# Performance work log

Measured on AMD Instinct MI355X. Metric: run time of the kernel, lower is better.

Reference implementation:

```python
import jax, jax.numpy as jnp
import numpy as np

B, T, D_IN, H, D_OUT = 256, 512, 64, 256, 8


def setup_inputs() -> dict:
    key = jax.random.key(0)
    ks = jax.random.split(key, 6)
    s_ih = 1.0 / np.sqrt(H)
    inputs = jax.random.normal(ks[0], (B, T, D_IN), dtype=jnp.float32)
    h0 = jnp.zeros((B, H), dtype=jnp.float32)
    c0 = jnp.zeros((B, H), dtype=jnp.float32)
    # LSTM cell params, PyTorch gate order (i, f, g, o)
    W_ih = jax.random.uniform(ks[1], (4 * H, D_IN), minval=-s_ih, maxval=s_ih, dtype=jnp.float32)
    W_hh = jax.random.uniform(ks[2], (4 * H, H), minval=-s_ih, maxval=s_ih, dtype=jnp.float32)
    b = jax.random.uniform(ks[3], (4 * H,), minval=-s_ih, maxval=s_ih, dtype=jnp.float32)
    # output projection (xavier_uniform weight, zero bias)
    lim = np.sqrt(6.0 / (H + D_OUT))
    W_out = jax.random.uniform(ks[4], (D_OUT, H), minval=-lim, maxval=lim, dtype=jnp.float32)
    b_out = jnp.zeros((D_OUT,), dtype=jnp.float32)
    return {"inputs": inputs, "h0": h0, "c0": c0, "W_ih": W_ih, "W_hh": W_hh,
            "b": b, "W_out": W_out, "b_out": b_out}


def _lstm_last(inputs, h0, c0, W_ih, W_hh, b):
    # inputs: [B, T, D_in] -> scan over time, keep only final hidden state
    xs = jnp.swapaxes(inputs, 0, 1)  # [T, B, D_in]

    def step(carry, x_t):
        h, c = carry
        gates = x_t @ W_ih.T + h @ W_hh.T + b  # [B, 4H]
        i, f, g, o = jnp.split(gates, 4, axis=-1)
        c_new = jax.nn.sigmoid(f) * c + jax.nn.sigmoid(i) * jnp.tanh(g)
        h_new = jax.nn.sigmoid(o) * jnp.tanh(c_new)
        return (h_new, c_new), None

    (h, c), _ = jax.lax.scan(step, (h0, c0), xs)
    return h, c


def reference(inputs, h0, c0, W_ih, W_hh, b, W_out, b_out):
    h, c = _lstm_last(inputs, h0, c0, W_ih, W_hh, b)
    rnn_outputs = h  # last-timestep output (dropout_prob=0 -> identity)
    logits = rnn_outputs @ W_out.T + b_out
    return (rnn_outputs, logits, h, c)
```

## Files before the change

### kernel.cpp

```cpp
#include <hip/hip_runtime.h>

#define T_ 512
#define B_ 256
#define H_ 256
#define DIN_ 64

typedef __attribute__((ext_vector_type(8))) short short8;
typedef __attribute__((ext_vector_type(4))) float f32x4;
typedef __attribute__((ext_vector_type(4))) unsigned int u32x4;

__device__ __forceinline__ unsigned short f2bf(float f) {
  unsigned u = __float_as_uint(f);
  u += 0x7FFFu + ((u >> 16) & 1u);
  return (unsigned short)(u >> 16);
}
__device__ __forceinline__ float bf2f(unsigned short s) {
  return __uint_as_float(((unsigned)s) << 16);
}
__device__ __forceinline__ float sigm(float x) { return 1.0f / (1.0f + __expf(-x)); }
__device__ __forceinline__ float tanh_(float x) {
  float xx = fminf(fmaxf(x, -30.0f), 30.0f);
  float e = __expf(2.0f * xx);
  return (e - 1.0f) / (e + 1.0f);
}

__device__ __forceinline__ void load4_sc1(const unsigned* p, u32x4& a) {
  asm volatile(
      "global_load_dwordx4 %0, %1, off sc1\n\t"
      "s_waitcnt vmcnt(0)"
      : "=&v"(a)
      : "v"(p) : "memory");
}

__device__ __forceinline__ bool tags_ok1(u32x4 a, unsigned w) {
  unsigned m = (a.x >> 16) ^ w; m |= (a.y >> 16) ^ w;
  m |= (a.z >> 16) ^ w;         m |= (a.w >> 16) ^ w;
  return m == 0;
}

__global__ __launch_bounds__(1024) void lstm_kern(
    const float* __restrict__ xin, const float* __restrict__ h0f,
    const float* __restrict__ c0f, const float* __restrict__ Wih,
    const float* __restrict__ Whh, const float* __restrict__ bias,
    const float* __restrict__ Wout, const float* __restrict__ bout,
    float* __restrict__ out, unsigned* hbuf32)
{
  const int tid = threadIdx.x;
  const int gb  = blockIdx.x & 15;
  const int gq  = blockIdx.x >> 4;
  const int wv  = tid >> 6;
  const int ln  = tid & 63;
  const int g   = wv & 3;
  const int hb  = wv >> 2;
  const int colB = ln & 15;
  const int krow = ln >> 4;

  __shared__ unsigned short h_s[16 * 264];
  __shared__ unsigned short x_s[16 * 72];
  __shared__ float gbuf[4 * 16 * 68];

  const int j = g * H_ + gq * 64 + hb * 16 + colB;
  short8 bh[8], bx[2];
  #pragma unroll
  for (int kc = 0; kc < 8; ++kc) {
    const float* p = Whh + j * H_ + kc * 32 + krow * 8;
    short8 f;
    #pragma unroll
    for (int i = 0; i < 8; ++i) f[i] = (short)f2bf(p[i]);
    bh[kc] = f;
  }
  #pragma unroll
  for (int kc = 0; kc < 2; ++kc) {
    const float* p = Wih + j * DIN_ + kc * 32 + krow * 8;
    short8 f;
    #pragma unroll
    for (int i = 0; i < 8; ++i) f[i] = (short)f2bf(p[i]);
    bx[kc] = f;
  }
  const float bval = bias[j];

  const int er = tid >> 6, ec = tid & 63;
  const int grow = gb * 16 + er;
  const int gcol = gq * 64 + ec;
  float c_val = c0f[grow * H_ + gcol];
  float h_val = 0.0f;

  const int xr = tid >> 4, xd = (tid & 15) * 4;
  const float* xrow = xin + (gb * 16 + (xr & 15)) * (T_ * DIN_) + xd;
  float4 xcur{};
  if (tid < 256) xcur = *(const float4*)(xrow);

  const int hr  = tid >> 6;
  const int hcb = (tid & 63) * 4;
  const unsigned* ldp_base = hbuf32 + gb * 4096 + hr * 256 + hcb;
  unsigned* stp_base = hbuf32 + gb * 4096 + er * 256 + gcol;

  for (int s = 1; s <= T_; ++s) {
    if (tid < 256) {
      unsigned short* q = &x_s[xr * 72 + xd];
      q[0] = f2bf(xcur.x); q[1] = f2bf(xcur.y);
      q[2] = f2bf(xcur.z); q[3] = f2bf(xcur.w);
      const int tn = (s < T_) ? s : (T_ - 1);
      xcur = *(const float4*)(xrow + tn * DIN_);
    }

    if (s == 1) {
      int r = tid >> 6, c4 = tid & 63;
      float4 v = ((const float4*)(h0f + (gb * 16 + r) * H_))[c4];
      unsigned short* q = &h_s[r * 264 + c4 * 4];
      q[0] = f2bf(v.x); q[1] = f2bf(v.y); q[2] = f2bf(v.z); q[3] = f2bf(v.w);
    } else {
      const unsigned want = (unsigned)(s - 1);
      const unsigned* ldp = ldp_base + (((s - 1) & 1) << 16);
      u32x4 va;
      int tries = 0;
      do {
        load4_sc1(ldp, va);
        if (tags_ok1(va, want)) break;
      } while (++tries < (1 << 18));
      unsigned* q32 = (unsigned*)&h_s[hr * 264 + hcb];
      q32[0] = (va.x & 0xFFFFu) | (va.y << 16);
      q32[1] = (va.z & 0xFFFFu) | (va.w << 16);
    }
    __syncthreads();

    f32x4 acc = {0.f, 0.f, 0.f, 0.f};
    #pragma unroll
    for (int kc = 0; kc < 2; ++kc) {
      short8 a = *(const short8*)&x_s[colB * 72 + kc * 32 + krow * 8];
      acc = __builtin_amdgcn_mfma_f32_16x16x32_bf16(a, bx[kc], acc, 0, 0, 0);
    }
    #pragma unroll
    for (int kc = 0; kc < 8; ++kc) {
      short8 a = *(const short8*)&h_s[colB * 264 + kc * 32 + krow * 8];
      acc = __builtin_amdgcn_mfma_f32_16x16x32_bf16(a, bh[kc], acc, 0, 0, 0);
    }
    #pragma unroll
    for (int i = 0; i < 4; ++i)
      gbuf[g * 1088 + (krow * 4 + i) * 68 + hb * 16 + colB] = acc[i] + bval;
    __syncthreads();

    float gi = gbuf[0 * 1088 + er * 68 + ec];
    float gf = gbuf[1 * 1088 + er * 68 + ec];
    float gg = gbuf[2 * 1088 + er * 68 + ec];
    float go = gbuf[3 * 1088 + er * 68 + ec];
    c_val = sigm(gf) * c_val + sigm(gi) * tanh_(gg);
    h_val = sigm(go) * tanh_(c_val);

    unsigned pk = ((unsigned)s << 16) | (unsigned)f2bf(h_val);
    __hip_atomic_store(stp_base + ((s & 1) << 16), pk,
                       __ATOMIC_RELAXED, __HIP_MEMORY_SCOPE_AGENT);
  }

  out[grow * H_ + gcol] = h_val;
  out[67584 + grow * H_ + gcol] = h_val;
  out[133120 + grow * H_ + gcol] = c_val;

  if (gq == 0) {
    const unsigned want = (unsigned)T_;
    const unsigned* ldp = ldp_base + ((T_ & 1) << 16);
    u32x4 va;
    int tries = 0;
    do {
      load4_sc1(ldp, va);
      if (tags_ok1(va, want)) break;
    } while (++tries < (1 << 18));
    unsigned* q32 = (unsigned*)&h_s[hr * 264 + hcb];
    q32[0] = (va.x & 0xFFFFu) | (va.y << 16);
    q32[1] = (va.z & 0xFFFFu) | (va.w << 16);
    __syncthreads();
    if (tid < 128) {
      int r = tid >> 3, o = tid & 7;
      float a = bout[o];
      for (int k = 0; k < H_; ++k)
        a = fmaf(bf2f(h_s[r * 264 + k]), Wout[o * H_ + k], a);
      out[65536 + (gb * 16 + r) * 8 + o] = a;
    }
  }
}

extern "C" void kernel_launch(void* const* d_in, const int* in_sizes, int n_in,
                              void* d_out, int out_size, void* d_ws, size_t ws_size,
                              hipStream_t stream) {
  const float* xin  = (const float*)d_in[0];
  const float* h0f  = (const float*)d_in[1];
  const float* c0f  = (const float*)d_in[2];
  const float* Wih  = (const float*)d_in[3];
  const float* Whh  = (const float*)d_in[4];
  const float* bias = (const float*)d_in[5];
  const float* Wout = (const float*)d_in[6];
  const float* bout = (const float*)d_in[7];
  float* out = (float*)d_out;

  unsigned* hbuf32 = (unsigned*)d_ws;

  void* args[] = {&xin, &h0f, &c0f, &Wih, &Whh, &bias, &Wout, &bout,
                  &out, &hbuf32};
  hipLaunchCooperativeKernel((void*)lstm_kern, dim3(64), dim3(1024),
                             args, 0, stream);
}
```

Before: 1.314 ms.

## Split hidden dimension across two blocks and overlap peer exchange with local MFMAs

Reworks the persistent LSTM kernel from 64 blocks of 1024 threads, each owning 64 hidden units, to 32 blocks of 512 threads, each owning 128 hidden units. Each wave now holds four gate tiles of weights in registers. Each block keeps its own half of h locally in LDS and only polls the partner block's half from global memory. The poll load is issued before the local-half MFMAs and waited on afterwards, hiding cross-block latency behind compute. This halves inter-block communication and sync participants but raises register pressure per thread (40 short8 weight fragments) and adds an extra __syncthreads per step.

```diff
diff --git a/kernel.cpp b/kernel.cpp
--- a/kernel.cpp
+++ b/kernel.cpp
@@ -24,152 +24,210 @@
   return (e - 1.0f) / (e + 1.0f);
 }
 
+__device__ __forceinline__ void poll_issue(const unsigned* p, u32x4& a) {
+  asm volatile("global_load_dwordx4 %0, %1, off sc1"
+               : "=&v"(a) : "v"(p) : "memory");
+}
+__device__ __forceinline__ void poll_wait(u32x4& a) {
+  asm volatile("s_waitcnt vmcnt(0)" : "+v"(a) :: "memory");
+}
 __device__ __forceinline__ void load4_sc1(const unsigned* p, u32x4& a) {
-  asm volatile(
-      "global_load_dwordx4 %0, %1, off sc1\n\t"
-      "s_waitcnt vmcnt(0)"
-      : "=&v"(a)
-      : "v"(p) : "memory");
-}
-
+  asm volatile("global_load_dwordx4 %0, %1, off sc1\n\t"
+               "s_waitcnt vmcnt(0)"
+               : "=&v"(a) : "v"(p) : "memory");
+}
 __device__ __forceinline__ bool tags_ok1(u32x4 a, unsigned w) {
   unsigned m = (a.x >> 16) ^ w; m |= (a.y >> 16) ^ w;
   m |= (a.z >> 16) ^ w;         m |= (a.w >> 16) ^ w;
   return m == 0;
 }
 
-__global__ __launch_bounds__(1024) void lstm_kern(
+__global__ __launch_bounds__(512, 2) void lstm_kern(
     const float* __restrict__ xin, const float* __restrict__ h0f,
     const float* __restrict__ c0f, const float* __restrict__ Wih,
     const float* __restrict__ Whh, const float* __restrict__ bias,
     const float* __restrict__ Wout, const float* __restrict__ bout,
     float* __restrict__ out, unsigned* hbuf32)
 {
-  const int tid = threadIdx.x;
-  const int gb  = blockIdx.x & 15;
-  const int gq  = blockIdx.x >> 4;
-  const int wv  = tid >> 6;
-  const int ln  = tid & 63;
-  const int g   = wv & 3;
-  const int hb  = wv >> 2;
+  const int tid  = threadIdx.x;
+  const int gb   = blockIdx.x & 15;
+  const int half = blockIdx.x >> 4;
+  const int ob   = half * 128;
+  const int pb   = 128 - ob;
+  const int wv   = tid >> 6;
+  const int ln   = tid & 63;
+  const int g    = wv & 3;
+  const int q    = wv >> 2;
   const int colB = ln & 15;
   const int krow = ln >> 4;
 
   __shared__ unsigned short h_s[16 * 264];
   __shared__ unsigned short x_s[16 * 72];
-  __shared__ float gbuf[4 * 16 * 68];
-
-  const int j = g * H_ + gq * 64 + hb * 16 + colB;
-  short8 bh[8], bx[2];
+  __shared__ float gbuf[4 * 16 * 132];
+
+  short8 bhw[4][8], bxw[4][2];
+  float bvw[4];
   #pragma unroll
-  for (int kc = 0; kc < 8; ++kc) {
-    const float* p = Whh + j * H_ + kc * 32 + krow * 8;
-    short8 f;
-    #pragma unroll
-    for (int i = 0; i < 8; ++i) f[i] = (short)f2bf(p[i]);
-    bh[kc] = f;
-  }
+  for (int jt = 0; jt < 4; ++jt) {
+    const int jr = g * H_ + ob + (q * 4 + jt) * 16 + colB;
+    #pragma unroll
+    for (int k = 0; k < 8; ++k) {
+      const int kcm = (half * 4 + k) & 7;
+      const float* p = Whh + jr * H_ + kcm * 32 + krow * 8;
+      short8 f;
+      #pragma unroll
+      for (int i = 0; i < 8; ++i) f[i] = (short)f2bf(p[i]);
+      bhw[jt][k] = f;
+    }
+    #pragma unroll
+    for (int kc = 0; kc < 2; ++kc) {
+      const float* p = Wih + jr * DIN_ + kc * 32 + krow * 8;
+      short8 f;
+      #pragma unroll
+      for (int i = 0; i < 8; ++i) f[i] = (short)f2bf(p[i]);
+      bxw[jt][kc] = f;
+    }
+    bvw[jt] = bias[jr];
+  }
+
+  const int crow = tid >> 5;
+  const int cl4  = (tid & 31) * 4;
+  const int grow = gb * 16 + crow;
+  const int gcol = ob + cl4;
+  float c_val[4], h_val[4];
   #pragma unroll
-  for (int kc = 0; kc < 2; ++kc) {
-    const float* p = Wih + j * DIN_ + kc * 32 + krow * 8;
-    short8 f;
-    #pragma unroll
-    for (int i = 0; i < 8; ++i) f[i] = (short)f2bf(p[i]);
-    bx[kc] = f;
-  }
-  const float bval = bias[j];
-
-  const int er = tid >> 6, ec = tid & 63;
-  const int grow = gb * 16 + er;
-  const int gcol = gq * 64 + ec;
-  float c_val = c0f[grow * H_ + gcol];
-  float h_val = 0.0f;
-
-  const int xr = tid >> 4, xd = (tid & 15) * 4;
-  const float* xrow = xin + (gb * 16 + (xr & 15)) * (T_ * DIN_) + xd;
-  float4 xcur{};
-  if (tid < 256) xcur = *(const float4*)(xrow);
-
-  const int hr  = tid >> 6;
-  const int hcb = (tid & 63) * 4;
-  const unsigned* ldp_base = hbuf32 + gb * 4096 + hr * 256 + hcb;
-  unsigned* stp_base = hbuf32 + gb * 4096 + er * 256 + gcol;
+  for (int i = 0; i < 4; ++i) {
+    c_val[i] = c0f[grow * H_ + gcol + i];
+    h_val[i] = 0.0f;
+  }
+
+  const int xr = tid >> 5, xc = (tid & 31) * 2;
+  const float* xrow = xin + (gb * 16 + xr) * (T_ * DIN_) + xc;
+  {
+    float2 v = *(const float2*)(xrow);
+    x_s[xr * 72 + xc]     = f2bf(v.x);
+    x_s[xr * 72 + xc + 1] = f2bf(v.y);
+  }
+  float2 xcur = *(const float2*)(xrow + DIN_);
+
+  {
+    const int r = tid >> 5, c8 = (tid & 31) * 8;
+    float4 v0 = *(const float4*)(h0f + (gb * 16 + r) * H_ + c8);
+    float4 v1 = *(const float4*)(h0f + (gb * 16 + r) * H_ + c8 + 4);
+    unsigned short* qq = &h_s[r * 264 + c8];
+    qq[0] = f2bf(v0.x); qq[1] = f2bf(v0.y); qq[2] = f2bf(v0.z); qq[3] = f2bf(v0.w);
+    qq[4] = f2bf(v1.x); qq[5] = f2bf(v1.y); qq[6] = f2bf(v1.z); qq[7] = f2bf(v1.w);
+  }
+
+  const int pr = tid >> 5, pc = pb + (tid & 31) * 4;
+  const unsigned* ldp_base = hbuf32 + gb * 4096 + pr * 256 + pc;
+  unsigned* stp_base = hbuf32 + gb * 4096 + crow * 256 + gcol;
+
+  __syncthreads();
 
   for (int s = 1; s <= T_; ++s) {
-    if (tid < 256) {
-      unsigned short* q = &x_s[xr * 72 + xd];
-      q[0] = f2bf(xcur.x); q[1] = f2bf(xcur.y);
-      q[2] = f2bf(xcur.z); q[3] = f2bf(xcur.w);
-      const int tn = (s < T_) ? s : (T_ - 1);
-      xcur = *(const float4*)(xrow + tn * DIN_);
-    }
-
-    if (s == 1) {
-      int r = tid >> 6, c4 = tid & 63;
-      float4 v = ((const float4*)(h0f + (gb * 16 + r) * H_))[c4];
-      unsigned short* q = &h_s[r * 264 + c4 * 4];
-      q[0] = f2bf(v.x); q[1] = f2bf(v.y); q[2] = f2bf(v.z); q[3] = f2bf(v.w);
-    } else {
-      const unsigned want = (unsigned)(s - 1);
-      const unsigned* ldp = ldp_base + (((s - 1) & 1) << 16);
-      u32x4 va;
-      int tries = 0;
-      do {
-        load4_sc1(ldp, va);
-        if (tags_ok1(va, want)) break;
-      } while (++tries < (1 << 18));
-      unsigned* q32 = (unsigned*)&h_s[hr * 264 + hcb];
-      q32[0] = (va.x & 0xFFFFu) | (va.y << 16);
-      q32[1] = (va.z & 0xFFFFu) | (va.w << 16);
-    }
-    __syncthreads();
-
-    f32x4 acc = {0.f, 0.f, 0.f, 0.f};
+    u32x4 pv;
+    const unsigned* ldp = ldp_base + (((s - 1) & 1) << 16);
+    if (s > 1) poll_issue(ldp, pv);
+
+    f32x4 acc[4] = {{0.f,0.f,0.f,0.f},{0.f,0.f,0.f,0.f},
+                    {0.f,0.f,0.f,0.f},{0.f,0.f,0.f,0.f}};
     #pragma unroll
     for (int kc = 0; kc < 2; ++kc) {
       short8 a = *(const short8*)&x_s[colB * 72 + kc * 32 + krow * 8];
-      acc = __builtin_amdgcn_mfma_f32_16x16x32_bf16(a, bx[kc], acc, 0, 0, 0);
-    }
-    #pragma unroll
-    for (int kc = 0; kc < 8; ++kc) {
-      short8 a = *(const short8*)&h_s[colB * 264 + kc * 32 + krow * 8];
-      acc = __builtin_amdgcn_mfma_f32_16x16x32_bf16(a, bh[kc], acc, 0, 0, 0);
-    }
-    #pragma unroll
-    for (int i = 0; i < 4; ++i)
-      gbuf[g * 1088 + (krow * 4 + i) * 68 + hb * 16 + colB] = acc[i] + bval;
-    __syncthreads();
-
-    float gi = gbuf[0 * 1088 + er * 68 + ec];
-    float gf = gbuf[1 * 1088 + er * 68 + ec];
-    float gg = gbuf[2 * 1088 + er * 68 + ec];
-    float go = gbuf[3 * 1088 + er * 68 + ec];
-    c_val = sigm(gf) * c_val + sigm(gi) * tanh_(gg);
-    h_val = sigm(go) * tanh_(c_val);
-
-    unsigned pk = ((unsigned)s << 16) | (unsigned)f2bf(h_val);
-    __hip_atomic_store(stp_base + ((s & 1) << 16), pk,
-                       __ATOMIC_RELAXED, __HIP_MEMORY_SCOPE_AGENT);
-  }
-
-  out[grow * H_ + gcol] = h_val;
-  out[67584 + grow * H_ + gcol] = h_val;
-  out[133120 + grow * H_ + gcol] = c_val;
-
-  if (gq == 0) {
+      #pragma unroll
+      for (int jt = 0; jt < 4; ++jt)
+        acc[jt] = __builtin_amdgcn_mfma_f32_16x16x32_bf16(a, bxw[jt][kc], acc[jt], 0, 0, 0);
+    }
+    #pragma unroll
+    for (int k = 0; k < 4; ++k) {
+      const int kcm = half * 4 + k;
+      short8 a = *(const short8*)&h_s[colB * 264 + kcm * 32 + krow * 8];
+      #pragma unroll
+      for (int jt = 0; jt < 4; ++jt)
+        acc[jt] = __builtin_amdgcn_mfma_f32_16x16x32_bf16(a, bhw[jt][k], acc[jt], 0, 0, 0);
+    }
+
+    if (s > 1) {
+      const unsigned want = (unsigned)(s - 1);
+      poll_wait(pv);
+      if (!tags_ok1(pv, want)) {
+        int tries = 0;
+        do {
+          load4_sc1(ldp, pv);
+          if (tags_ok1(pv, want)) break;
+        } while (++tries < (1 << 18));
+      }
+      unsigned* q32 = (unsigned*)&h_s[pr * 264 + pc];
+      q32[0] = (pv.x & 0xFFFFu) | (pv.y << 16);
+      q32[1] = (pv.z & 0xFFFFu) | (pv.w << 16);
+    }
+    __syncthreads();
+
+    #pragma unroll
+    for (int k = 4; k < 8; ++k) {
+      const int kcm = (half * 4 + k) & 7;
+      short8 a = *(const short8*)&h_s[colB * 264 + kcm * 32 + krow * 8];
+      #pragma unroll
+      for (int jt = 0; jt < 4; ++jt)
+        acc[jt] = __builtin_amdgcn_mfma_f32_16x16x32_bf16(a, bhw[jt][k], acc[jt], 0, 0, 0);
+    }
+    #pragma unroll
+    for (int jt = 0; jt < 4; ++jt) {
+      const int gc0 = (q * 4 + jt) * 16 + colB;
+      #pragma unroll
+      for (int i = 0; i < 4; ++i)
+        gbuf[g * 2112 + (krow * 4 + i) * 132 + gc0] = acc[jt][i] + bvw[jt];
+    }
+    __syncthreads();
+
+    {
+      const f32x4 vi = *(const f32x4*)&gbuf[0 * 2112 + crow * 132 + cl4];
+      const f32x4 vf = *(const f32x4*)&gbuf[1 * 2112 + crow * 132 + cl4];
+      const f32x4 vg = *(const f32x4*)&gbuf[2 * 2112 + crow * 132 + cl4];
+      const f32x4 vo = *(const f32x4*)&gbuf[3 * 2112 + crow * 132 + cl4];
+      unsigned short* hq = &h_s[crow * 264 + gcol];
+      unsigned* st = stp_base + ((s & 1) << 16);
+      #pragma unroll
+      for (int i = 0; i < 4; ++i) {
+        c_val[i] = sigm(vf[i]) * c_val[i] + sigm(vi[i]) * tanh_(vg[i]);
+        h_val[i] = sigm(vo[i]) * tanh_(c_val[i]);
+        unsigned short hb = f2bf(h_val[i]);
+        hq[i] = hb;
+        __hip_atomic_store(st + i, ((unsigned)s << 16) | (unsigned)hb,
+                           __ATOMIC_RELAXED, __HIP_MEMORY_SCOPE_AGENT);
+      }
+    }
+    x_s[xr * 72 + xc]     = f2bf(xcur.x);
+    x_s[xr * 72 + xc + 1] = f2bf(xcur.y);
+    {
+      const int tn = (s + 1 < T_) ? (s + 1) : (T_ - 1);
+      xcur = *(const float2*)(xrow + tn * DIN_);
+    }
+    __syncthreads();
+  }
+
+  #pragma unroll
+  for (int i = 0; i < 4; ++i) {
+    out[grow * H_ + gcol + i]          = h_val[i];
+    out[67584 + grow * H_ + gcol + i]  = h_val[i];
+    out[133120 + grow * H_ + gcol + i] = c_val[i];
+  }
+
+  {
     const unsigned want = (unsigned)T_;
     const unsigned* ldp = ldp_base + ((T_ & 1) << 16);
-    u32x4 va;
+    u32x4 pv;
     int tries = 0;
     do {
-      load4_sc1(ldp, va);
-      if (tags_ok1(va, want)) break;
+      load4_sc1(ldp, pv);
+      if (tags_ok1(pv, want)) break;
     } while (++tries < (1 << 18));
-    unsigned* q32 = (unsigned*)&h_s[hr * 264 + hcb];
-    q32[0] = (va.x & 0xFFFFu) | (va.y << 16);
-    q32[1] = (va.z & 0xFFFFu) | (va.w << 16);
-    __syncthreads();
-    if (tid < 128) {
+    unsigned* q32 = (unsigned*)&h_s[pr * 264 + pc];
+    q32[0] = (pv.x & 0xFFFFu) | (pv.y << 16);
+    q32[1] = (pv.z & 0xFFFFu) | (pv.w << 16);
+    __syncthreads();
+    if (half == 0 && tid < 128) {
       int r = tid >> 3, o = tid & 7;
       float a = bout[o];
       for (int k = 0; k < H_; ++k)
@@ -196,6 +254,6 @@
 
   void* args[] = {&xin, &h0f, &c0f, &Wih, &Whh, &bias, &Wout, &bout,
                   &out, &hbuf32};
-  hipLaunchCooperativeKernel((void*)lstm_kern, dim3(64), dim3(1024),
+  hipLaunchCooperativeKernel((void*)lstm_kern, dim3(32), dim3(512),
                              args, 0, stream);
 }
```

New measurement: 1.435 ms. +9.2%, slower.
